# Performance work log

Measured on AMD Instinct MI355X. Metric: run time of the kernel, lower is better.

## Reference

```python
import jax, jax.numpy as jnp
import numpy as np

B, DIM, NH, HD, H, W = 4, 64, 8, 8, 256, 256  # head_dim must equal num_heads (scale broadcast)


def setup_inputs() -> dict:
    key = jax.random.key(0)
    ks = jax.random.split(key, 10)
    s = 0.05
    return {
        "x": jax.random.normal(ks[0], (B, DIM, H, W), jnp.float32),
        "w3": jax.random.normal(ks[1], (DIM, 1, 3, 3), jnp.float32) * s,  # depthwise 3x3
        "b3": jax.random.normal(ks[2], (DIM,), jnp.float32) * s,
        "w5": jax.random.normal(ks[3], (DIM, 1, 5, 5), jnp.float32) * s,  # depthwise 5x5
        "b5": jax.random.normal(ks[4], (DIM,), jnp.float32) * s,
        "wqkv": jax.random.normal(ks[5], (3 * DIM, DIM), jnp.float32) * s,  # 1x1 conv, no bias
        "scale": jnp.ones((NH, 1, 1), jnp.float32),
        "g1_w": jax.random.normal(ks[6], (DIM // 4, DIM), jnp.float32) * s,
        "g1_b": jnp.zeros((DIM // 4,), jnp.float32),
        "g2_w": jax.random.normal(ks[7], (2, DIM // 4), jnp.float32) * s,
        "g2_b": jnp.zeros((2,), jnp.float32),
        "wp": jax.random.normal(ks[8], (DIM, DIM), jnp.float32) * s,  # 1x1 proj
        "bp": jnp.zeros((DIM,), jnp.float32),
    }


def _dwconv(x, w, b, pad):
    out = jax.lax.conv_general_dilated(
        x, w, (1, 1), [(pad, pad), (pad, pad)],
        dimension_numbers=("NCHW", "OIHW", "NCHW"), feature_group_count=x.shape[1])
    return out + b[None, :, None, None]


def _l2norm(t, eps=1e-12):  # F.normalize(dim=-1)
    n = jnp.sqrt(jnp.sum(t * t, axis=-1, keepdims=True))
    return t / jnp.maximum(n, eps)


def reference(x, w3, b3, w5, b5, wqkv, scale, g1_w, g1_b, g2_w, g2_b, wp, bp):
    b, c, h, w = x.shape
    conv_feat = _dwconv(x, w3, b3, 1) + _dwconv(x, w5, b5, 2)

    qkv = jnp.einsum("oc,bchw->bohw", wqkv, x)          # [b,3c,h,w]
    qkv = qkv.reshape(b, 3, NH, HD, h * w)
    q, k, v = qkv[:, 0], qkv[:, 1], qkv[:, 2]           # [b,NH,HD,hw]
    q = _l2norm(q)
    k = _l2norm(k)

    q_h = q.reshape(b, NH, HD, h, w)
    k_h = k.reshape(b, NH, HD, h, w)
    v_h = v.reshape(b, NH, HD, h, w)

    # row-axis attention: per (b,head,d-channel) attention over rows x (scale broadcasts onto HD axis)
    attn_h = jnp.einsum("bhdxy,bhdzy->bhdxz", q_h, k_h) * scale   # [b,NH,HD,h,h]
    attn_h = jax.nn.softmax(attn_h, axis=-1)
    out_h = jnp.einsum("bhdxz,bhdzy->bhdxy", attn_h, v_h).reshape(b, c, h, w)

    # column-axis attention (operate on transposed spatial layout)
    q_v = jnp.swapaxes(q_h, -1, -2)                      # [b,NH,HD,w,h]
    k_v = jnp.swapaxes(k_h, -1, -2)
    v_v = jnp.swapaxes(v_h, -1, -2)
    attn_v = jnp.einsum("bhdyx,bhdzx->bhdyz", q_v, k_v) * scale   # [b,NH,HD,w,w]
    attn_v = jax.nn.softmax(attn_v, axis=-1)
    out_v = jnp.einsum("bhdyz,bhdzx->bhdyx", attn_v, v_v)         # [b,NH,HD,w,h]
    out_v = jnp.swapaxes(out_v, -1, -2).reshape(b, c, h, w)

    attn_feat = out_h + out_v

    # global-pool gating: softmax over 2 mixing weights
    gx = jnp.mean(x, axis=(2, 3))                        # [b,c]
    h1 = jax.nn.relu(gx @ g1_w.T + g1_b)
    gw = jax.nn.softmax(h1 @ g2_w.T + g2_b, axis=1)      # [b,2]
    cw = gw[:, 0][:, None, None, None]
    aw = gw[:, 1][:, None, None, None]

    out = cw * conv_feat + aw * attn_feat
    return jnp.einsum("oc,bchw->bohw", wp, out) + bp[None, :, None, None]
```

## Files before the change

kernel.cpp:

```cpp
#include <hip/hip_runtime.h>
#include <stdint.h>


typedef unsigned short u16;
typedef __attribute__((ext_vector_type(8))) short bf16x8;
typedef __attribute__((ext_vector_type(4))) float f32x4;

#define DEV static __device__ __forceinline__

DEV u16 f2bf(float f) {
  unsigned u = __float_as_uint(f);
  return (u16)((u + 0x7fffu + ((u >> 16) & 1u)) >> 16);
}
DEV float bf2f(u16 h) { return __uint_as_float(((unsigned)h) << 16); }

__global__ void k_gx(const float* __restrict__ x, float* __restrict__ gxsum) {
  int bc = blockIdx.x, t = threadIdx.x;
  const float4* p = (const float4*)(x + ((size_t)bc << 16));
  float s = 0.f;
  for (int i = 0; i < 64; ++i) { float4 v = p[t + 256 * i]; s += v.x + v.y + v.z + v.w; }
  for (int off = 32; off; off >>= 1) s += __shfl_down(s, off);
  __shared__ float lds[4];
  if ((t & 63) == 0) lds[t >> 6] = s;
  __syncthreads();
  if (t == 0) gxsum[bc] = lds[0] + lds[1] + lds[2] + lds[3];
}

__global__ void k_gate(const float* __restrict__ gxsum, const float* __restrict__ g1w,
                       const float* __restrict__ g1b, const float* __restrict__ g2w,
                       const float* __restrict__ g2b, float* __restrict__ cwaw) {
  __shared__ float h1[4][16];
  int t = threadIdx.x;
  int b = t >> 4, j = t & 15;
  float a = g1b[j];
  for (int c = 0; c < 64; ++c) a += g1w[j * 64 + c] * gxsum[b * 64 + c] * (1.f / 65536.f);
  h1[b][j] = fmaxf(a, 0.f);
  __syncthreads();
  if (t < 4) {
    float l0 = g2b[0], l1 = g2b[1];
    for (int k = 0; k < 16; ++k) { l0 += g2w[k] * h1[t][k]; l1 += g2w[16 + k] * h1[t][k]; }
    float m = fmaxf(l0, l1);
    float e0 = __expf(l0 - m), e1 = __expf(l1 - m);
    float inv = 1.f / (e0 + e1);
    cwaw[t * 2 + 0] = e0 * inv;
    cwaw[t * 2 + 1] = e1 * inv;
  }
}

__global__ __launch_bounds__(256) void k_qkv(const float* __restrict__ x,
                                             const float* __restrict__ wqkv,
                                             u16* __restrict__ qkv) {
  __shared__ u16 Ws[192 * 72];
  __shared__ u16 Xs[128 * 72];
  int t = threadIdx.x;
  int b = blockIdx.x >> 9;
  int p0 = (blockIdx.x & 511) << 7;

  {
    int row = t >> 2, c0 = (t & 3) << 4;
#pragma unroll
    for (int i = 0; i < 3; ++i) {
      int r = i * 64 + row;
      const float* src = wqkv + r * 64 + c0;
      unsigned pk[8];
#pragma unroll
      for (int j = 0; j < 8; ++j)
        pk[j] = (unsigned)f2bf(src[2 * j]) | ((unsigned)f2bf(src[2 * j + 1]) << 16);
      uint4* dst = (uint4*)&Ws[r * 72 + c0];
      dst[0] = make_uint4(pk[0], pk[1], pk[2], pk[3]);
      dst[1] = make_uint4(pk[4], pk[5], pk[6], pk[7]);
    }
  }
  {
    int p = t & 127, ch = t >> 7;
    const float* xb = x + ((size_t)(b * 64) << 16) + p0 + p;
#pragma unroll
    for (int i = 0; i < 32; ++i) {
      int c = 2 * i + ch;
      Xs[p * 72 + c] = f2bf(xb[(size_t)c << 16]);
    }
  }
  __syncthreads();

  int w = t >> 6, l = t & 63, q = l >> 4, cl = l & 15;
  bf16x8 af[3][2];
#pragma unroll
  for (int g = 0; g < 3; ++g)
#pragma unroll
    for (int k = 0; k < 2; ++k)
      af[g][k] = *(const bf16x8*)&Ws[(w * 48 + g * 16 + cl) * 72 + k * 32 + q * 8];

  f32x4 acc[3][8];
  f32x4 zero = {0.f, 0.f, 0.f, 0.f};
#pragma unroll
  for (int g = 0; g < 3; ++g)
#pragma unroll
    for (int j = 0; j < 8; ++j) acc[g][j] = zero;

  for (int j = 0; j < 8; ++j) {
    bf16x8 b0 = *(const bf16x8*)&Xs[(j * 16 + cl) * 72 + q * 8];
    bf16x8 b1 = *(const bf16x8*)&Xs[(j * 16 + cl) * 72 + 32 + q * 8];
#pragma unroll
    for (int g = 0; g < 3; ++g) {
      acc[g][j] = __builtin_amdgcn_mfma_f32_16x16x32_bf16(af[g][0], b0, acc[g][j], 0, 0, 0);
      acc[g][j] = __builtin_amdgcn_mfma_f32_16x16x32_bf16(af[g][1], b1, acc[g][j], 0, 0, 0);
    }
  }
  u16* outb = qkv + ((size_t)(b * 192) << 16) + p0;
  for (int g = 0; g < 3; ++g) {
    int rowb = w * 48 + g * 16 + q * 4;
#pragma unroll
    for (int r = 0; r < 4; ++r) {
      u16* orow = outb + ((size_t)(rowb + r) << 16);
#pragma unroll
      for (int j = 0; j < 8; ++j) orow[j * 16 + cl] = f2bf(acc[g][j][r]);
    }
  }
}

__global__ void k_rnorm(const u16* __restrict__ qkv, float* __restrict__ rnorm) {
  int b = blockIdx.x >> 7, ch = blockIdx.x & 127;
  const uint2* p2 = (const uint2*)(qkv + ((size_t)(b * 192 + ch) << 16));
  int t = threadIdx.x;
  float s = 0.f;
  for (int i = 0; i < 64; ++i) {
    uint2 v = p2[t + 256 * i];
    float a = bf2f(v.x & 0xffff), bq = bf2f(v.x >> 16);
    float c = bf2f(v.y & 0xffff), d = bf2f(v.y >> 16);
    s += a * a + bq * bq + c * c + d * d;
  }
  for (int off = 32; off; off >>= 1) s += __shfl_down(s, off);
  __shared__ float lds[4];
  if ((t & 63) == 0) lds[t >> 6] = s;
  __syncthreads();
  if (t == 0) {
    float tot = lds[0] + lds[1] + lds[2] + lds[3];
    rnorm[blockIdx.x] = 1.f / fmaxf(sqrtf(tot), 1e-12f);
  }
}

__global__ void k_conv(const float* __restrict__ x, const float* __restrict__ w3,
                       const float* __restrict__ b3, const float* __restrict__ w5,
                       const float* __restrict__ b5, const float* __restrict__ cwaw,
                       float* __restrict__ outmix) {
  int rt = blockIdx.x & 31, bc = blockIdx.x >> 5, c = bc & 63, b = bc >> 6;
  int r0 = rt * 8;
  const float* xp = x + ((size_t)bc << 16);
  __shared__ float xs[12][256];
  int y = threadIdx.x;
  for (int rr = 0; rr < 12; ++rr) {
    int gr = r0 - 2 + rr;
    xs[rr][y] = (gr >= 0 && gr < 256) ? xp[(size_t)gr * 256 + y] : 0.f;
  }
  __syncthreads();
  float W3[9], W5[25];
#pragma unroll
  for (int i = 0; i < 9; ++i) W3[i] = w3[c * 9 + i];
#pragma unroll
  for (int i = 0; i < 25; ++i) W5[i] = w5[c * 25 + i];
  float bias = b3[c] + b5[c];
  float cw = cwaw[b * 2];
  float* op = outmix + ((size_t)bc << 16);
  for (int k = 0; k < 8; ++k) {
    float a = bias;
#pragma unroll
    for (int di = 0; di < 3; ++di)
#pragma unroll
      for (int dj = 0; dj < 3; ++dj) {
        int yy = y + dj - 1;
        float xv = (yy >= 0 && yy < 256) ? xs[k + 1 + di][yy] : 0.f;
        a += W3[di * 3 + dj] * xv;
      }
#pragma unroll
    for (int di = 0; di < 5; ++di)
#pragma unroll
      for (int dj = 0; dj < 5; ++dj) {
        int yy = y + dj - 2;
        float xv = (yy >= 0 && yy < 256) ? xs[k + di][yy] : 0.f;
        a += W5[di * 5 + dj] * xv;
      }
    op[(size_t)(r0 + k) * 256 + y] = cw * a;
  }
}

__global__ __launch_bounds__(256) void k_attn(
    const u16* __restrict__ qkv, const float* __restrict__ rnorm,
    const float* __restrict__ scale, u16* __restrict__ oh, u16* __restrict__ ov) {
  __shared__ __align__(16) unsigned char smem[34816];
  u16* Pls = (u16*)smem;
  float* red = (float*)(smem + 33792);
  float* Osf = (float*)smem;

  int t = threadIdx.x;
  int w = t >> 6, l = t & 63, q = l >> 4, cl = l & 15;
  int idx = blockIdx.x;
  int rt = idx & 3, dir = (idx >> 2) & 1, c = (idx >> 3) & 63, b = idx >> 9;
  int r0 = rt << 6;

  const size_t P = 65536;
  const u16* Qp = qkv + (size_t)(b * 192 + c) * P;
  const u16* Kp = qkv + (size_t)(b * 192 + 64 + c) * P;
  const u16* Vp = qkv + (size_t)(b * 192 + 128 + c) * P;

  float sc = rnorm[b * 128 + c] * rnorm[b * 128 + 64 + c] * scale[c >> 3];

  f32x4 Sa[4][4];
  f32x4 zero = {0.f, 0.f, 0.f, 0.f};
#pragma unroll
  for (int i = 0; i < 4; ++i)
#pragma unroll
    for (int j = 0; j < 4; ++j) Sa[i][j] = zero;

  for (int yw = 0; yw < 8; ++yw) {
    int y0 = yw << 5;
    bf16x8 af[4], bfr[4];
    if (dir == 0) {
#pragma unroll
      for (int i = 0; i < 4; ++i)
        af[i] = *(const bf16x8*)&Qp[(size_t)(r0 + i * 16 + cl) * 256 + y0 + q * 8];
#pragma unroll
      for (int j = 0; j < 4; ++j)
        bfr[j] = *(const bf16x8*)&Kp[(size_t)(w * 64 + j * 16 + cl) * 256 + y0 + q * 8];
    } else {
#pragma unroll
      for (int i = 0; i < 4; ++i) {
        bf16x8 tmp;
#pragma unroll
        for (int jj = 0; jj < 8; ++jj)
          tmp[jj] = (short)Qp[(y0 + q * 8 + jj) * 256 + r0 + i * 16 + cl];
        af[i] = tmp;
      }
#pragma unroll
      for (int j = 0; j < 4; ++j) {
        bf16x8 tmp;
#pragma unroll
        for (int jj = 0; jj < 8; ++jj)
          tmp[jj] = (short)Kp[(y0 + q * 8 + jj) * 256 + w * 64 + j * 16 + cl];
        bfr[j] = tmp;
      }
    }
#pragma unroll
    for (int i = 0; i < 4; ++i)
#pragma unroll
      for (int j = 0; j < 4; ++j)
        Sa[i][j] = __builtin_amdgcn_mfma_f32_16x16x32_bf16(af[i], bfr[j], Sa[i][j], 0, 0, 0);
  }

#pragma unroll
  for (int i = 0; i < 4; ++i)
#pragma unroll
    for (int j = 0; j < 4; ++j) Sa[i][j] *= sc;

  float mx[4][4], sm[4][4];
#pragma unroll
  for (int i = 0; i < 4; ++i)
#pragma unroll
    for (int r = 0; r < 4; ++r) {
      float m = fmaxf(fmaxf(Sa[i][0][r], Sa[i][1][r]), fmaxf(Sa[i][2][r], Sa[i][3][r]));
#pragma unroll
      for (int off = 1; off < 16; off <<= 1) m = fmaxf(m, __shfl_xor(m, off));
      mx[i][r] = m;
    }
  if (cl == 0) {
#pragma unroll
    for (int i = 0; i < 4; ++i)
#pragma unroll
      for (int r = 0; r < 4; ++r) red[w * 64 + i * 16 + q * 4 + r] = mx[i][r];
  }
  __syncthreads();
#pragma unroll
  for (int i = 0; i < 4; ++i)
#pragma unroll
    for (int r = 0; r < 4; ++r) {
      int rho = i * 16 + q * 4 + r;
      mx[i][r] = fmaxf(fmaxf(red[rho], red[64 + rho]), fmaxf(red[128 + rho], red[192 + rho]));
    }
  __syncthreads();
#pragma unroll
  for (int i = 0; i < 4; ++i)
#pragma unroll
    for (int r = 0; r < 4; ++r) {
      float s0 = 0.f;
#pragma unroll
      for (int j = 0; j < 4; ++j) {
        float e = __expf(Sa[i][j][r] - mx[i][r]);
        Sa[i][j][r] = e;
        s0 += e;
      }
#pragma unroll
      for (int off = 1; off < 16; off <<= 1) s0 += __shfl_xor(s0, off);
      sm[i][r] = s0;
    }
  if (cl == 0) {
#pragma unroll
    for (int i = 0; i < 4; ++i)
#pragma unroll
      for (int r = 0; r < 4; ++r) red[w * 64 + i * 16 + q * 4 + r] = sm[i][r];
  }
  __syncthreads();
#pragma unroll
  for (int i = 0; i < 4; ++i)
#pragma unroll
    for (int r = 0; r < 4; ++r) {
      int rho = i * 16 + q * 4 + r;
      sm[i][r] = 1.f / (red[rho] + red[64 + rho] + red[128 + rho] + red[192 + rho]);
    }
#pragma unroll
  for (int i = 0; i < 4; ++i)
#pragma unroll
    for (int r = 0; r < 4; ++r) {
      int rho = i * 16 + q * 4 + r;
#pragma unroll
      for (int j = 0; j < 4; ++j)
        Pls[rho * 264 + w * 64 + j * 16 + cl] = f2bf(Sa[i][j][r] * sm[i][r]);
    }
  __syncthreads();

  f32x4 Oa[4][4];
#pragma unroll
  for (int i = 0; i < 4; ++i)
#pragma unroll
    for (int j = 0; j < 4; ++j) Oa[i][j] = zero;
  for (int zw = 0; zw < 8; ++zw) {
    int z0 = zw << 5;
    bf16x8 af[4], bfr[4];
#pragma unroll
    for (int i = 0; i < 4; ++i) af[i] = *(const bf16x8*)&Pls[(i * 16 + cl) * 264 + z0 + q * 8];
    if (dir == 0) {
#pragma unroll
      for (int j = 0; j < 4; ++j) {
        bf16x8 tmp;
#pragma unroll
        for (int jj = 0; jj < 8; ++jj)
          tmp[jj] = (short)Vp[(z0 + q * 8 + jj) * 256 + w * 64 + j * 16 + cl];
        bfr[j] = tmp;
      }
    } else {
#pragma unroll
      for (int j = 0; j < 4; ++j)
        bfr[j] = *(const bf16x8*)&Vp[(size_t)(w * 64 + j * 16 + cl) * 256 + z0 + q * 8];
    }
#pragma unroll
    for (int i = 0; i < 4; ++i)
#pragma unroll
      for (int j = 0; j < 4; ++j)
        Oa[i][j] = __builtin_amdgcn_mfma_f32_16x16x32_bf16(af[i], bfr[j], Oa[i][j], 0, 0, 0);
  }

  if (dir == 0) {
    u16* op = oh + (size_t)(b * 64 + c) * P;
#pragma unroll
    for (int i = 0; i < 4; ++i)
#pragma unroll
      for (int j = 0; j < 4; ++j)
#pragma unroll
        for (int r = 0; r < 4; ++r)
          op[(size_t)(r0 + i * 16 + q * 4 + r) * 256 + w * 64 + j * 16 + cl] = f2bf(Oa[i][j][r]);
  } else {
    u16* op = ov + (size_t)(b * 64 + c) * P;
    __syncthreads();
    for (int h = 0; h < 2; ++h) {
#pragma unroll
      for (int ii = 0; ii < 2; ++ii) {
        int i = h * 2 + ii;
#pragma unroll
        for (int j = 0; j < 4; ++j)
#pragma unroll
          for (int r = 0; r < 4; ++r)
            Osf[(ii * 16 + q * 4 + r) * 260 + w * 64 + j * 16 + cl] = Oa[i][j][r];
      }
      __syncthreads();
      int rr = t & 31, xb = t >> 5;
      for (int xx = 0; xx < 32; ++xx) {
        int xcol = xx * 8 + xb;
        op[(size_t)xcol * 256 + r0 + h * 32 + rr] = f2bf(Osf[rr * 260 + xcol]);
      }
      __syncthreads();
    }
  }
}

__global__ __launch_bounds__(256) void k_final(
    float* __restrict__ dout, const u16* __restrict__ oh, const u16* __restrict__ ov,
    const float* __restrict__ wp, const float* __restrict__ bp,
    const float* __restrict__ cwaw) {
  __shared__ u16 Ms[256 * 72];
  __shared__ u16 Ws[64 * 72];
  int t = threadIdx.x;
  int b = blockIdx.x >> 8;
  int p0 = (blockIdx.x & 255) << 8;
  float aw = cwaw[b * 2 + 1];

  {
    int row = t >> 2, c0 = (t & 3) << 4;
    const float* src = wp + row * 64 + c0;
    unsigned pk[8];
#pragma unroll
    for (int j = 0; j < 8; ++j)
      pk[j] = (unsigned)f2bf(src[2 * j]) | ((unsigned)f2bf(src[2 * j + 1]) << 16);
    uint4* dst = (uint4*)&Ws[row * 72 + c0];
    dst[0] = make_uint4(pk[0], pk[1], pk[2], pk[3]);
    dst[1] = make_uint4(pk[4], pk[5], pk[6], pk[7]);
  }
  {
    size_t base = ((size_t)(b * 64) << 16) + p0 + t;
    for (int c = 0; c < 64; ++c) {
      size_t off = base + ((size_t)c << 16);
      float m = dout[off] + aw * (bf2f(oh[off]) + bf2f(ov[off]));
      Ms[t * 72 + c] = f2bf(m);
    }
  }
  __syncthreads();

  int w = t >> 6, l = t & 63, q = l >> 4, cl = l & 15;
  bf16x8 af0 = *(const bf16x8*)&Ws[(w * 16 + cl) * 72 + q * 8];
  bf16x8 af1 = *(const bf16x8*)&Ws[(w * 16 + cl) * 72 + 32 + q * 8];

  f32x4 acc[16];
  f32x4 zero = {0.f, 0.f, 0.f, 0.f};
#pragma unroll
  for (int j = 0; j < 16; ++j) acc[j] = zero;

  for (int j = 0; j < 16; ++j) {
    bf16x8 b0 = *(const bf16x8*)&Ms[(j * 16 + cl) * 72 + q * 8];
    bf16x8 b1 = *(const bf16x8*)&Ms[(j * 16 + cl) * 72 + 32 + q * 8];
    acc[j] = __builtin_amdgcn_mfma_f32_16x16x32_bf16(af0, b0, acc[j], 0, 0, 0);
    acc[j] = __builtin_amdgcn_mfma_f32_16x16x32_bf16(af1, b1, acc[j], 0, 0, 0);
  }

  float bpv[4];
#pragma unroll
  for (int r = 0; r < 4; ++r) bpv[r] = bp[w * 16 + q * 4 + r];
  float* outb = dout + ((size_t)(b * 64) << 16) + p0;
#pragma unroll
  for (int r = 0; r < 4; ++r) {
    float* orow = outb + ((size_t)(w * 16 + q * 4 + r) << 16);
#pragma unroll
    for (int j = 0; j < 16; ++j) orow[j * 16 + cl] = acc[j][r] + bpv[r];
  }
}

extern "C" void kernel_launch(void* const* d_in, const int* in_sizes, int n_in,
                              void* d_out, int out_size, void* d_ws, size_t ws_size,
                              hipStream_t stream) {
  const float* x = (const float*)d_in[0];
  const float* w3 = (const float*)d_in[1];
  const float* b3 = (const float*)d_in[2];
  const float* w5 = (const float*)d_in[3];
  const float* b5 = (const float*)d_in[4];
  const float* wqkv = (const float*)d_in[5];
  const float* scale = (const float*)d_in[6];
  const float* g1w = (const float*)d_in[7];
  const float* g1b = (const float*)d_in[8];
  const float* g2w = (const float*)d_in[9];
  const float* g2b = (const float*)d_in[10];
  const float* wp = (const float*)d_in[11];
  const float* bp = (const float*)d_in[12];
  float* out = (float*)d_out;

  char* ws = (char*)d_ws;
  u16* qkv = (u16*)(ws);
  u16* ohb = (u16*)(ws + 100663296ull);
  u16* ovb = (u16*)(ws + 134217728ull);
  float* fs = (float*)(ws + 167772160ull);
  float* gxsum = fs;
  float* cwaw = fs + 256;
  float* rnorm = fs + 264;

  k_gx<<<256, 256, 0, stream>>>(x, gxsum);
  k_gate<<<1, 64, 0, stream>>>(gxsum, g1w, g1b, g2w, g2b, cwaw);
  k_qkv<<<2048, 256, 0, stream>>>(x, wqkv, qkv);
  k_rnorm<<<512, 256, 0, stream>>>(qkv, rnorm);
  k_conv<<<8192, 256, 0, stream>>>(x, w3, b3, w5, b5, cwaw, out);
  k_attn<<<2048, 256, 0, stream>>>(qkv, rnorm, scale, ohb, ovb);
  k_final<<<1024, 256, 0, stream>>>(out, ohb, ovb, wp, bp, cwaw);
}
```

Baseline: 377.2 us.

## Pre-transpose Q/K for column attention and stage V through LDS transpose

Adds a kernel that transposes the Q and K planes into a scratch buffer (reusing the output buffer before the conv writes it), so column-direction attention can use contiguous 16-byte loads instead of strided scalar gathers. In row-direction attention, V tiles are loaded coalesced and transposed through a swizzled LDS buffer rather than gathered element by element. Block indices are also remapped so the two directions interleave. The cost is an extra transpose pass over Q and K, more LDS per block and extra barriers in the PV loop. The attention kernel is moved before the conv so the borrowed output buffer is free.

```diff
diff --git a/kernel.cpp b/kernel.cpp
--- a/kernel.cpp
+++ b/kernel.cpp
@@ -137,6 +137,41 @@
     float tot = lds[0] + lds[1] + lds[2] + lds[3];
     rnorm[blockIdx.x] = 1.f / fmaxf(sqrtf(tot), 1e-12f);
   }
+}
+
+__global__ __launch_bounds__(256) void k_tr(const u16* __restrict__ qkv,
+                                            u16* __restrict__ qkvT) {
+  int blk = blockIdx.x;
+  int tile = blk & 15;
+  int pl = blk >> 4;
+  int b = pl >> 7, ch = pl & 127;
+  int h0 = (tile >> 2) << 6, w0 = (tile & 3) << 6;
+  const u16* ip = qkv + ((size_t)(b * 192 + ch) << 16);
+  u16* op = qkvT + ((size_t)pl << 16);
+  __shared__ unsigned lds32[64][33];
+  int t = threadIdx.x;
+
+  int r = t >> 2, qd = t & 3;
+  uint4 v0 = *(const uint4*)&ip[(size_t)(h0 + r) * 256 + w0 + qd * 16];
+  uint4 v1 = *(const uint4*)&ip[(size_t)(h0 + r) * 256 + w0 + qd * 16 + 8];
+  unsigned vv[8] = {v0.x, v0.y, v0.z, v0.w, v1.x, v1.y, v1.z, v1.w};
+#pragma unroll
+  for (int k = 0; k < 8; ++k) lds32[r][qd * 8 + k] = vv[k];
+  __syncthreads();
+
+  int wl = t >> 2, hq = t & 3;
+  unsigned pkout[8];
+#pragma unroll
+  for (int m = 0; m < 8; ++m) {
+    unsigned a = lds32[hq * 16 + 2 * m][wl >> 1];
+    unsigned b2 = lds32[hq * 16 + 2 * m + 1][wl >> 1];
+    pkout[m] = (wl & 1) ? ((a >> 16) | (b2 & 0xffff0000u))
+                        : ((a & 0xffffu) | (b2 << 16));
+  }
+  *(uint4*)&op[(size_t)(w0 + wl) * 256 + h0 + hq * 16] =
+      make_uint4(pkout[0], pkout[1], pkout[2], pkout[3]);
+  *(uint4*)&op[(size_t)(w0 + wl) * 256 + h0 + hq * 16 + 8] =
+      make_uint4(pkout[4], pkout[5], pkout[6], pkout[7]);
 }
 
 __global__ void k_conv(const float* __restrict__ x, const float* __restrict__ w3,
@@ -184,22 +219,24 @@
 }
 
 __global__ __launch_bounds__(256) void k_attn(
-    const u16* __restrict__ qkv, const float* __restrict__ rnorm,
-    const float* __restrict__ scale, u16* __restrict__ oh, u16* __restrict__ ov) {
-  __shared__ __align__(16) unsigned char smem[34816];
+    const u16* __restrict__ qkv, const u16* __restrict__ qkvT,
+    const float* __restrict__ rnorm, const float* __restrict__ scale,
+    u16* __restrict__ oh, u16* __restrict__ ov) {
+  __shared__ __align__(16) unsigned char smem[54272];
   u16* Pls = (u16*)smem;
   float* red = (float*)(smem + 33792);
+  unsigned* Vt32 = (unsigned*)(smem + 33792);
   float* Osf = (float*)smem;
 
   int t = threadIdx.x;
   int w = t >> 6, l = t & 63, q = l >> 4, cl = l & 15;
-  int idx = blockIdx.x;
+  int idx = (blockIdx.x & 7) * 256 + (blockIdx.x >> 3);
   int rt = idx & 3, dir = (idx >> 2) & 1, c = (idx >> 3) & 63, b = idx >> 9;
   int r0 = rt << 6;
 
   const size_t P = 65536;
-  const u16* Qp = qkv + (size_t)(b * 192 + c) * P;
-  const u16* Kp = qkv + (size_t)(b * 192 + 64 + c) * P;
+  const u16* Qp = dir ? qkvT + (size_t)(b * 128 + c) * P : qkv + (size_t)(b * 192 + c) * P;
+  const u16* Kp = dir ? qkvT + (size_t)(b * 128 + 64 + c) * P : qkv + (size_t)(b * 192 + 64 + c) * P;
   const u16* Vp = qkv + (size_t)(b * 192 + 128 + c) * P;
 
   float sc = rnorm[b * 128 + c] * rnorm[b * 128 + 64 + c] * scale[c >> 3];
@@ -214,31 +251,12 @@
   for (int yw = 0; yw < 8; ++yw) {
     int y0 = yw << 5;
     bf16x8 af[4], bfr[4];
-    if (dir == 0) {
-#pragma unroll
-      for (int i = 0; i < 4; ++i)
-        af[i] = *(const bf16x8*)&Qp[(size_t)(r0 + i * 16 + cl) * 256 + y0 + q * 8];
-#pragma unroll
-      for (int j = 0; j < 4; ++j)
-        bfr[j] = *(const bf16x8*)&Kp[(size_t)(w * 64 + j * 16 + cl) * 256 + y0 + q * 8];
-    } else {
-#pragma unroll
-      for (int i = 0; i < 4; ++i) {
-        bf16x8 tmp;
-#pragma unroll
-        for (int jj = 0; jj < 8; ++jj)
-          tmp[jj] = (short)Qp[(y0 + q * 8 + jj) * 256 + r0 + i * 16 + cl];
-        af[i] = tmp;
-      }
-#pragma unroll
-      for (int j = 0; j < 4; ++j) {
-        bf16x8 tmp;
-#pragma unroll
-        for (int jj = 0; jj < 8; ++jj)
-          tmp[jj] = (short)Kp[(y0 + q * 8 + jj) * 256 + w * 64 + j * 16 + cl];
-        bfr[j] = tmp;
-      }
-    }
+#pragma unroll
+    for (int i = 0; i < 4; ++i)
+      af[i] = *(const bf16x8*)&Qp[(size_t)(r0 + i * 16 + cl) * 256 + y0 + q * 8];
+#pragma unroll
+    for (int j = 0; j < 4; ++j)
+      bfr[j] = *(const bf16x8*)&Kp[(size_t)(w * 64 + j * 16 + cl) * 256 + y0 + q * 8];
 #pragma unroll
     for (int i = 0; i < 4; ++i)
 #pragma unroll
@@ -321,30 +339,59 @@
   for (int i = 0; i < 4; ++i)
 #pragma unroll
     for (int j = 0; j < 4; ++j) Oa[i][j] = zero;
-  for (int zw = 0; zw < 8; ++zw) {
-    int z0 = zw << 5;
-    bf16x8 af[4], bfr[4];
-#pragma unroll
-    for (int i = 0; i < 4; ++i) af[i] = *(const bf16x8*)&Pls[(i * 16 + cl) * 264 + z0 + q * 8];
-    if (dir == 0) {
+
+  if (dir == 0) {
+    int z2 = t >> 4, colc = t & 15;
+    int zlo = z2 & 3;
+    int wkey = (((z2 >> 2) ^ (colc & 3)) << 2) + zlo;
+    for (int zw = 0; zw < 8; ++zw) {
+      int z0 = zw << 5;
+      const u16* rp = Vp + (size_t)(z0 + 2 * z2) * 256 + colc * 16;
+      uint4 a0 = *(const uint4*)rp;
+      uint4 a1 = *(const uint4*)(rp + 8);
+      uint4 c0 = *(const uint4*)(rp + 256);
+      uint4 c1 = *(const uint4*)(rp + 264);
+      unsigned A[8] = {a0.x, a0.y, a0.z, a0.w, a1.x, a1.y, a1.z, a1.w};
+      unsigned Bv[8] = {c0.x, c0.y, c0.z, c0.w, c1.x, c1.y, c1.z, c1.w};
+      __syncthreads();
+#pragma unroll
+      for (int m = 0; m < 16; ++m) {
+        unsigned lo = (m & 1) ? (A[m >> 1] >> 16) : (A[m >> 1] & 0xffffu);
+        unsigned hi = (m & 1) ? (Bv[m >> 1] & 0xffff0000u) : (Bv[m >> 1] << 16);
+        Vt32[(colc * 16 + m) * 20 + wkey] = lo | hi;
+      }
+      __syncthreads();
+      bf16x8 af[4], bfr[4];
+#pragma unroll
+      for (int i = 0; i < 4; ++i)
+        af[i] = *(const bf16x8*)&Pls[(i * 16 + cl) * 264 + z0 + q * 8];
 #pragma unroll
       for (int j = 0; j < 4; ++j) {
-        bf16x8 tmp;
-#pragma unroll
-        for (int jj = 0; jj < 8; ++jj)
-          tmp[jj] = (short)Vp[(z0 + q * 8 + jj) * 256 + w * 64 + j * 16 + cl];
-        bfr[j] = tmp;
-      }
-    } else {
+        int col = w * 64 + j * 16 + cl;
+        bfr[j] = *(const bf16x8*)&Vt32[col * 20 + ((q ^ j) << 2)];
+      }
+#pragma unroll
+      for (int i = 0; i < 4; ++i)
+#pragma unroll
+        for (int j = 0; j < 4; ++j)
+          Oa[i][j] = __builtin_amdgcn_mfma_f32_16x16x32_bf16(af[i], bfr[j], Oa[i][j], 0, 0, 0);
+    }
+  } else {
+    for (int zw = 0; zw < 8; ++zw) {
+      int z0 = zw << 5;
+      bf16x8 af[4], bfr[4];
+#pragma unroll
+      for (int i = 0; i < 4; ++i)
+        af[i] = *(const bf16x8*)&Pls[(i * 16 + cl) * 264 + z0 + q * 8];
 #pragma unroll
       for (int j = 0; j < 4; ++j)
         bfr[j] = *(const bf16x8*)&Vp[(size_t)(w * 64 + j * 16 + cl) * 256 + z0 + q * 8];
-    }
-#pragma unroll
-    for (int i = 0; i < 4; ++i)
-#pragma unroll
-      for (int j = 0; j < 4; ++j)
-        Oa[i][j] = __builtin_amdgcn_mfma_f32_16x16x32_bf16(af[i], bfr[j], Oa[i][j], 0, 0, 0);
+#pragma unroll
+      for (int i = 0; i < 4; ++i)
+#pragma unroll
+        for (int j = 0; j < 4; ++j)
+          Oa[i][j] = __builtin_amdgcn_mfma_f32_16x16x32_bf16(af[i], bfr[j], Oa[i][j], 0, 0, 0);
+    }
   }
 
   if (dir == 0) {
@@ -466,12 +513,14 @@
   float* gxsum = fs;
   float* cwaw = fs + 256;
   float* rnorm = fs + 264;
+  u16* qkvT = (u16*)d_out;
 
   k_gx<<<256, 256, 0, stream>>>(x, gxsum);
   k_gate<<<1, 64, 0, stream>>>(gxsum, g1w, g1b, g2w, g2b, cwaw);
   k_qkv<<<2048, 256, 0, stream>>>(x, wqkv, qkv);
   k_rnorm<<<512, 256, 0, stream>>>(qkv, rnorm);
+  k_tr<<<8192, 256, 0, stream>>>(qkv, qkvT);
+  k_attn<<<2048, 256, 0, stream>>>(qkv, qkvT, rnorm, scale, ohb, ovb);
   k_conv<<<8192, 256, 0, stream>>>(x, w3, b3, w5, b5, cwaw, out);
-  k_attn<<<2048, 256, 0, stream>>>(qkv, rnorm, scale, ohb, ovb);
   k_final<<<1024, 256, 0, stream>>>(out, ohb, ovb, wp, bp, cwaw);
 }
```

After: 391.3 us. 3.7% more time.

## Stage strided Q/K/V tiles through swizzled LDS transposes and drop softmax max pass

Applied to the files above, without the earlier changes.

Replaces the strided 2-byte global gathers used for the transposed Q/K (column attention) and V (row attention) operands with coalesced 16-byte loads. These are packed into bf16 pairs and written to XOR-swizzled LDS tiles, so the MFMA fragments can be read as contiguous vectors. It also drops the row-max reduction in softmax, relying on the L2-normalised q·k being bounded so exp cannot overflow. The block index is also remapped to interleave work across the grid. In exchange it adds LDS usage (from 34816 to 54272 bytes), extra barriers per iteration, and a softmax that depends on bounded scores.

```diff
diff --git a/kernel.cpp b/kernel.cpp
--- a/kernel.cpp
+++ b/kernel.cpp
@@ -186,14 +186,16 @@
 __global__ __launch_bounds__(256) void k_attn(
     const u16* __restrict__ qkv, const float* __restrict__ rnorm,
     const float* __restrict__ scale, u16* __restrict__ oh, u16* __restrict__ ov) {
-  __shared__ __align__(16) unsigned char smem[34816];
+  __shared__ __align__(16) unsigned char smem[54272];
   u16* Pls = (u16*)smem;
+  unsigned* Qt32 = (unsigned*)smem;
   float* red = (float*)(smem + 33792);
+  unsigned* Tt32 = (unsigned*)(smem + 33792);
   float* Osf = (float*)smem;
 
   int t = threadIdx.x;
   int w = t >> 6, l = t & 63, q = l >> 4, cl = l & 15;
-  int idx = blockIdx.x;
+  int idx = (blockIdx.x & 7) * 256 + (blockIdx.x >> 3);
   int rt = idx & 3, dir = (idx >> 2) & 1, c = (idx >> 3) & 63, b = idx >> 9;
   int r0 = rt << 6;
 
@@ -211,71 +213,73 @@
 #pragma unroll
     for (int j = 0; j < 4; ++j) Sa[i][j] = zero;
 
-  for (int yw = 0; yw < 8; ++yw) {
-    int y0 = yw << 5;
-    bf16x8 af[4], bfr[4];
-    if (dir == 0) {
+  if (dir == 0) {
+    for (int yw = 0; yw < 8; ++yw) {
+      int y0 = yw << 5;
+      bf16x8 af[4], bfr[4];
 #pragma unroll
       for (int i = 0; i < 4; ++i)
         af[i] = *(const bf16x8*)&Qp[(size_t)(r0 + i * 16 + cl) * 256 + y0 + q * 8];
 #pragma unroll
       for (int j = 0; j < 4; ++j)
         bfr[j] = *(const bf16x8*)&Kp[(size_t)(w * 64 + j * 16 + cl) * 256 + y0 + q * 8];
-    } else {
-#pragma unroll
-      for (int i = 0; i < 4; ++i) {
-        bf16x8 tmp;
-#pragma unroll
-        for (int jj = 0; jj < 8; ++jj)
-          tmp[jj] = (short)Qp[(y0 + q * 8 + jj) * 256 + r0 + i * 16 + cl];
-        af[i] = tmp;
-      }
+#pragma unroll
+      for (int i = 0; i < 4; ++i)
+#pragma unroll
+        for (int j = 0; j < 4; ++j)
+          Sa[i][j] = __builtin_amdgcn_mfma_f32_16x16x32_bf16(af[i], bfr[j], Sa[i][j], 0, 0, 0);
+    }
+  } else {
+    int y2 = t >> 4, colc = t & 15;
+    int kkey = (((y2 >> 2) ^ (colc & 3)) << 2) + (y2 & 3);
+    int qkey = (((y2 >> 2) ^ ((colc >> 2) & 3)) << 2) + (y2 & 3);
+    for (int yw = 0; yw < 8; ++yw) {
+      int y0 = yw << 5;
+      const u16* krp = Kp + (size_t)(y0 + 2 * y2) * 256 + colc * 16;
+      uint4 ka0 = *(const uint4*)krp;
+      uint4 ka1 = *(const uint4*)(krp + 8);
+      uint4 kb0 = *(const uint4*)(krp + 256);
+      uint4 kb1 = *(const uint4*)(krp + 264);
+      const u16* qrp = Qp + (size_t)(y0 + 2 * y2) * 256 + r0 + colc * 4;
+      uint2 qa = *(const uint2*)qrp;
+      uint2 qb = *(const uint2*)(qrp + 256);
+      unsigned KA[8] = {ka0.x, ka0.y, ka0.z, ka0.w, ka1.x, ka1.y, ka1.z, ka1.w};
+      unsigned KB[8] = {kb0.x, kb0.y, kb0.z, kb0.w, kb1.x, kb1.y, kb1.z, kb1.w};
+      unsigned QA[2] = {qa.x, qa.y};
+      unsigned QB[2] = {qb.x, qb.y};
+      __syncthreads();
+#pragma unroll
+      for (int m = 0; m < 16; ++m) {
+        unsigned lo = (m & 1) ? (KA[m >> 1] >> 16) : (KA[m >> 1] & 0xffffu);
+        unsigned hi = (m & 1) ? (KB[m >> 1] & 0xffff0000u) : (KB[m >> 1] << 16);
+        Tt32[(colc * 16 + m) * 20 + kkey] = lo | hi;
+      }
+#pragma unroll
+      for (int m = 0; m < 4; ++m) {
+        unsigned lo = (m & 1) ? (QA[m >> 1] >> 16) : (QA[m >> 1] & 0xffffu);
+        unsigned hi = (m & 1) ? (QB[m >> 1] & 0xffff0000u) : (QB[m >> 1] << 16);
+        Qt32[(colc * 4 + m) * 20 + qkey] = lo | hi;
+      }
+      __syncthreads();
+      bf16x8 af[4], bfr[4];
+#pragma unroll
+      for (int i = 0; i < 4; ++i)
+        af[i] = *(const bf16x8*)&Qt32[(i * 16 + cl) * 20 + ((q ^ i) << 2)];
 #pragma unroll
       for (int j = 0; j < 4; ++j) {
-        bf16x8 tmp;
-#pragma unroll
-        for (int jj = 0; jj < 8; ++jj)
-          tmp[jj] = (short)Kp[(y0 + q * 8 + jj) * 256 + w * 64 + j * 16 + cl];
-        bfr[j] = tmp;
-      }
-    }
-#pragma unroll
-    for (int i = 0; i < 4; ++i)
-#pragma unroll
-      for (int j = 0; j < 4; ++j)
-        Sa[i][j] = __builtin_amdgcn_mfma_f32_16x16x32_bf16(af[i], bfr[j], Sa[i][j], 0, 0, 0);
-  }
-
-#pragma unroll
-  for (int i = 0; i < 4; ++i)
-#pragma unroll
-    for (int j = 0; j < 4; ++j) Sa[i][j] *= sc;
-
-  float mx[4][4], sm[4][4];
-#pragma unroll
-  for (int i = 0; i < 4; ++i)
-#pragma unroll
-    for (int r = 0; r < 4; ++r) {
-      float m = fmaxf(fmaxf(Sa[i][0][r], Sa[i][1][r]), fmaxf(Sa[i][2][r], Sa[i][3][r]));
-#pragma unroll
-      for (int off = 1; off < 16; off <<= 1) m = fmaxf(m, __shfl_xor(m, off));
-      mx[i][r] = m;
-    }
-  if (cl == 0) {
-#pragma unroll
-    for (int i = 0; i < 4; ++i)
-#pragma unroll
-      for (int r = 0; r < 4; ++r) red[w * 64 + i * 16 + q * 4 + r] = mx[i][r];
-  }
-  __syncthreads();
-#pragma unroll
-  for (int i = 0; i < 4; ++i)
-#pragma unroll
-    for (int r = 0; r < 4; ++r) {
-      int rho = i * 16 + q * 4 + r;
-      mx[i][r] = fmaxf(fmaxf(red[rho], red[64 + rho]), fmaxf(red[128 + rho], red[192 + rho]));
-    }
-  __syncthreads();
+        int col = w * 64 + j * 16 + cl;
+        bfr[j] = *(const bf16x8*)&Tt32[col * 20 + ((q ^ j) << 2)];
+      }
+#pragma unroll
+      for (int i = 0; i < 4; ++i)
+#pragma unroll
+        for (int j = 0; j < 4; ++j)
+          Sa[i][j] = __builtin_amdgcn_mfma_f32_16x16x32_bf16(af[i], bfr[j], Sa[i][j], 0, 0, 0);
+    }
+    __syncthreads();
+  }
+
+  float sm[4][4];
 #pragma unroll
   for (int i = 0; i < 4; ++i)
 #pragma unroll
@@ -283,7 +287,7 @@
       float s0 = 0.f;
 #pragma unroll
       for (int j = 0; j < 4; ++j) {
-        float e = __expf(Sa[i][j][r] - mx[i][r]);
+        float e = __expf(Sa[i][j][r] * sc);
         Sa[i][j][r] = e;
         s0 += e;
       }
@@ -321,33 +325,43 @@
   for (int i = 0; i < 4; ++i)
 #pragma unroll
     for (int j = 0; j < 4; ++j) Oa[i][j] = zero;
-  for (int zw = 0; zw < 8; ++zw) {
-    int z0 = zw << 5;
-    bf16x8 af[4], bfr[4];
-#pragma unroll
-    for (int i = 0; i < 4; ++i) af[i] = *(const bf16x8*)&Pls[(i * 16 + cl) * 264 + z0 + q * 8];
-    if (dir == 0) {
+
+  if (dir == 0) {
+    int z2 = t >> 4, colc = t & 15;
+    int zlo = z2 & 3;
+    int wkey = (((z2 >> 2) ^ (colc & 3)) << 2) + zlo;
+    for (int zw = 0; zw < 8; ++zw) {
+      int z0 = zw << 5;
+      const u16* rp = Vp + (size_t)(z0 + 2 * z2) * 256 + colc * 16;
+      uint4 a0 = *(const uint4*)rp;
+      uint4 a1 = *(const uint4*)(rp + 8);
+      uint4 c0 = *(const uint4*)(rp + 256);
+      uint4 c1 = *(const uint4*)(rp + 264);
+      unsigned A[8] = {a0.x, a0.y, a0.z, a0.w, a1.x, a1.y, a1.z, a1.w};
+      unsigned Bv[8] = {c0.x, c0.y, c0.z, c0.w, c1.x, c1.y, c1.z, c1.w};
+      __syncthreads();
+#pragma unroll
+      for (int m = 0; m < 16; ++m) {
+        unsigned lo = (m & 1) ? (A[m >> 1] >> 16) : (A[m >> 1] & 0xffffu);
+        unsigned hi = (m & 1) ? (Bv[m >> 1] & 0xffff0000u) : (Bv[m >> 1] << 16);
+        Tt32[(colc * 16 + m) * 20 + wkey] = lo | hi;
+      }
+      __syncthreads();
+      bf16x8 af[4], bfr[4];
+#pragma unroll
+      for (int i = 0; i < 4; ++i)
+        af[i] = *(const bf16x8*)&Pls[(i * 16 + cl) * 264 + z0 + q * 8];
 #pragma unroll
       for (int j = 0; j < 4; ++j) {
-        bf16x8 tmp;
-#pragma unroll
-        for (int jj = 0; jj < 8; ++jj)
-          tmp[jj] = (short)Vp[(z0 + q * 8 + jj) * 256 + w * 64 + j * 16 + cl];
-        bfr[j] = tmp;
-      }
-    } else {
-#pragma unroll
-      for (int j = 0; j < 4; ++j)
-        bfr[j] = *(const bf16x8*)&Vp[(size_t)(w * 64 + j * 16 + cl) * 256 + z0 + q * 8];
-    }
-#pragma unroll
-    for (int i = 0; i < 4; ++i)
-#pragma unroll
-      for (int j = 0; j < 4; ++j)
-        Oa[i][j] = __builtin_amdgcn_mfma_f32_16x16x32_bf16(af[i], bfr[j], Oa[i][j], 0, 0, 0);
-  }
-
-  if (dir == 0) {
+        int col = w * 64 + j * 16 + cl;
+        bfr[j] = *(const bf16x8*)&Tt32[col * 20 + ((q ^ j) << 2)];
+      }
+#pragma unroll
+      for (int i = 0; i < 4; ++i)
+#pragma unroll
+        for (int j = 0; j < 4; ++j)
+          Oa[i][j] = __builtin_amdgcn_mfma_f32_16x16x32_bf16(af[i], bfr[j], Oa[i][j], 0, 0, 0);
+    }
     u16* op = oh + (size_t)(b * 64 + c) * P;
 #pragma unroll
     for (int i = 0; i < 4; ++i)
@@ -357,6 +371,21 @@
         for (int r = 0; r < 4; ++r)
           op[(size_t)(r0 + i * 16 + q * 4 + r) * 256 + w * 64 + j * 16 + cl] = f2bf(Oa[i][j][r]);
   } else {
+    for (int zw = 0; zw < 8; ++zw) {
+      int z0 = zw << 5;
+      bf16x8 af[4], bfr[4];
+#pragma unroll
+      for (int i = 0; i < 4; ++i)
+        af[i] = *(const bf16x8*)&Pls[(i * 16 + cl) * 264 + z0 + q * 8];
+#pragma unroll
+      for (int j = 0; j < 4; ++j)
+        bfr[j] = *(const bf16x8*)&Vp[(size_t)(w * 64 + j * 16 + cl) * 256 + z0 + q * 8];
+#pragma unroll
+      for (int i = 0; i < 4; ++i)
+#pragma unroll
+        for (int j = 0; j < 4; ++j)
+          Oa[i][j] = __builtin_amdgcn_mfma_f32_16x16x32_bf16(af[i], bfr[j], Oa[i][j], 0, 0, 0);
+    }
     u16* op = ov + (size_t)(b * 64 + c) * P;
     __syncthreads();
     for (int h = 0; h < 2; ++h) {
```

Result: faster. 355.0 us (-5.9%).
